# Kernel tuning notes

Measured on AMD Instinct MI355X. Metric: run time of the kernel, lower is better.

Reference implementation:

```python
import jax, jax.numpy as jnp
import numpy as np

B, L, D = 4, 16384, 128          # batch, voxels per sample, d_model
DI, DS, DTR, K = 256, 16, 8, 4   # d_inner, d_state, dt_rank, conv kernel
N = B * L
EPS = 1e-5


def setup_inputs() -> dict:
    key = jax.random.key(0)
    ks = jax.random.split(key, 12)
    s = 0.02
    feats = jax.random.normal(ks[0], (N, D), jnp.float32)
    coords_xyz = jax.random.randint(ks[1], (N, 3), 0, 1024, jnp.int32)
    # per-batch Morton permutation + its inverse
    perm = jnp.stack([jax.random.permutation(jax.random.fold_in(ks[2], i), L) for i in range(B)]).astype(jnp.int32)
    inv_perm = jnp.argsort(perm, axis=1).astype(jnp.int32)
    return {
        'feats': feats,
        'pos_w': jax.random.normal(ks[3], (3, D), jnp.float32) * s,
        'pos_b': jnp.zeros((D,), jnp.float32),
        'rms_w': jnp.ones((D,), jnp.float32),
        'in_proj_w': jax.random.normal(ks[4], (D, 2 * DI), jnp.float32) * s,
        'conv_w': jax.random.normal(ks[5], (DI, K), jnp.float32) * s,
        'conv_b': jnp.zeros((DI,), jnp.float32),
        'x_proj_w': jax.random.normal(ks[6], (DI, DTR + 2 * DS), jnp.float32) * s,
        'dt_proj_w': jax.random.normal(ks[7], (DTR, DI), jnp.float32) * s,
        'dt_proj_b': jax.random.normal(ks[8], (DI,), jnp.float32) * 0.1,
        'A_log': jnp.log(jnp.broadcast_to(jnp.arange(1.0, DS + 1.0, dtype=jnp.float32), (DI, DS))),
        'D_param': jnp.ones((DI,), jnp.float32),
        'out_proj_w': jax.random.normal(ks[9], (DI, D), jnp.float32) * s,
        'ln_w': jnp.ones((D,), jnp.float32),
        'ln_b': jnp.zeros((D,), jnp.float32),
        'coords_xyz': coords_xyz,
        'perm': perm,
        'inv_perm': inv_perm,
    }


def _gssm(feats, pos_w, pos_b, rms_w, in_proj_w, conv_w, conv_b, x_proj_w,
          dt_proj_w, dt_proj_b, A_log, D_param, out_proj_w, ln_w, ln_b,
          coords_xyz, perm, inv_perm):
    # positional embedding of voxel coords
    pe = coords_xyz.astype(jnp.float32) @ pos_w + pos_b            # [N, D]
    h = (feats + pe).reshape(B, L, D)
    # gather into Morton order (per-batch fancy index)
    hm = jnp.take_along_axis(h, perm[:, :, None].astype(jnp.int32), axis=1)  # [B, L, D]
    # Mamba block: RMSNorm then mixer (block returns mixer output only)
    x = hm * jax.lax.rsqrt(jnp.mean(hm * hm, axis=-1, keepdims=True) + EPS) * rms_w
    xz = x @ in_proj_w                                             # [B, L, 2*DI]
    xi, z = xz[..., :DI], xz[..., DI:]
    # depthwise causal conv1d, kernel K
    xp = jnp.pad(xi, ((0, 0), (K - 1, 0), (0, 0)))
    xc = conv_b + sum(xp[:, j:j + L, :] * conv_w[:, j] for j in range(K))
    xc = jax.nn.silu(xc)                                           # [B, L, DI]
    dbc = xc @ x_proj_w                                            # [B, L, DTR+2*DS]
    dt, Bm, Cm = dbc[..., :DTR], dbc[..., DTR:DTR + DS], dbc[..., DTR + DS:]
    dt = jax.nn.softplus(dt @ dt_proj_w + dt_proj_b)               # [B, L, DI]
    A = -jnp.exp(A_log)                                            # [DI, DS]

    def step(hst, inp):
        x_t, dt_t, b_t, c_t = inp                                  # [B,DI],[B,DI],[B,DS],[B,DS]
        hst = jnp.exp(dt_t[..., None] * A) * hst + (dt_t * x_t)[..., None] * b_t[:, None, :]
        return hst, jnp.einsum('bds,bs->bd', hst, c_t)

    h0 = jnp.zeros((B, DI, DS), xc.dtype)
    _, ys = jax.lax.scan(step, h0, (xc.transpose(1, 0, 2), dt.transpose(1, 0, 2),
                                    Bm.transpose(1, 0, 2), Cm.transpose(1, 0, 2)))
    y = ys.transpose(1, 0, 2) + xc * D_param                       # [B, L, DI]
    y = y * jax.nn.silu(z)
    out = y @ out_proj_w                                           # [B, L, D]
    # scatter back to original voxel order
    out = jnp.take_along_axis(out, inv_perm[:, :, None].astype(jnp.int32), axis=1).reshape(N, D)
    # post-SSM LayerNorm
    mu = jnp.mean(out, axis=-1, keepdims=True)
    var = jnp.mean((out - mu) ** 2, axis=-1, keepdims=True)
    return (out - mu) * jax.lax.rsqrt(var + EPS) * ln_w + ln_b


def reference(feats, pos_w, pos_b, rms_w, in_proj_w, conv_w, conv_b, x_proj_w,
              dt_proj_w, dt_proj_b, A_log, D_param, out_proj_w, ln_w, ln_b,
              coords_xyz, perm, inv_perm):
    return _gssm(feats, pos_w, pos_b, rms_w, in_proj_w, conv_w, conv_b, x_proj_w,
                 dt_proj_w, dt_proj_b, A_log, D_param, out_proj_w, ln_w, ln_b,
                 coords_xyz, perm, inv_perm)
```

## Files before the change

kernel.cpp:

```cpp
#include <hip/hip_runtime.h>
#include <hip/hip_bf16.h>
#include <math.h>

#define B_   4
#define L_   16384
#define D_   128
#define DI_  256
#define DS_  16
#define DTR_ 8
#define N_   65536
#define NC_  128
#define LC_  128
#define TW_  16
#define TP_  260
#define EPS_ 1e-5f

typedef __hip_bfloat16 bf16;
typedef __attribute__((ext_vector_type(8))) short short8;
typedef __attribute__((ext_vector_type(4))) float f32x4;

__device__ __forceinline__ bool probe_bf16(const void* Dp) {
  return ((const unsigned*)Dp)[0] == 0x3F803F80u;
}
__device__ __forceinline__ float ldin(const void* p, size_t i, bool isb) {
  return isb ? __bfloat162float(((const bf16*)p)[i]) : ((const float*)p)[i];
}
__device__ __forceinline__ float4 ld4(const void* p, size_t i4, bool isb) {
  if (!isb) return ((const float4*)p)[i4];
  const ushort4 v = ((const ushort4*)p)[i4];
  float4 r;
  r.x = __uint_as_float((unsigned)v.x << 16);
  r.y = __uint_as_float((unsigned)v.y << 16);
  r.z = __uint_as_float((unsigned)v.z << 16);
  r.w = __uint_as_float((unsigned)v.w << 16);
  return r;
}
__device__ __forceinline__ void splitbf(float v, ushort& hi, ushort& lo) {
  bf16 h = __float2bfloat16(v);
  float rem = v - __bfloat162float(h);
  bf16 l = __float2bfloat16(rem);
  hi = *(ushort*)&h;
  lo = *(ushort*)&l;
}


__global__ __launch_bounds__(256) void k_xnorm(
    const void* __restrict__ feats, const void* __restrict__ pos_w,
    const void* __restrict__ pos_b, const void* __restrict__ rms_w,
    const int* __restrict__ coords, const int* __restrict__ perm,
    const void* __restrict__ Dprobe,
    ushort* __restrict__ xh, ushort* __restrict__ xl) {
  const bool isb = probe_bf16(Dprobe);
  int wv = threadIdx.x >> 6, lane = threadIdx.x & 63;
  int p = blockIdx.x * 4 + wv;
  int b = p >> 14;
  int srow = b * L_ + perm[p];
  float cx = (float)coords[srow*3+0];
  float cy = (float)coords[srow*3+1];
  float cz = (float)coords[srow*3+2];
  int i0 = lane, i1 = lane + 64;
  float h0 = ldin(feats,(size_t)srow*D_ + i0,isb) + cx*ldin(pos_w,i0,isb) + cy*ldin(pos_w,D_+i0,isb)
           + cz*ldin(pos_w,2*D_+i0,isb) + ldin(pos_b,i0,isb);
  float h1 = ldin(feats,(size_t)srow*D_ + i1,isb) + cx*ldin(pos_w,i1,isb) + cy*ldin(pos_w,D_+i1,isb)
           + cz*ldin(pos_w,2*D_+i1,isb) + ldin(pos_b,i1,isb);
  float ss = h0*h0 + h1*h1;
  #pragma unroll
  for (int off = 32; off; off >>= 1) ss += __shfl_xor(ss, off);
  float r = 1.0f / sqrtf(ss * (1.f/128.f) + EPS_);
  float v0 = h0 * r * ldin(rms_w,i0,isb);
  float v1 = h1 * r * ldin(rms_w,i1,isb);
  ushort a, bq;
  splitbf(v0, a, bq);
  xh[(size_t)p*D_ + i0] = a; xl[(size_t)p*D_ + i0] = bq;
  splitbf(v1, a, bq);
  xh[(size_t)p*D_ + i1] = a; xl[(size_t)p*D_ + i1] = bq;
}

__global__ __launch_bounds__(256) void k_prepw(
    const void* __restrict__ Win, const void* __restrict__ Dprobe,
    ushort* __restrict__ wth, ushort* __restrict__ wtl) {
  const bool isb = probe_bf16(Dprobe);
  int idx = blockIdx.x * 256 + threadIdx.x;
  int k = idx >> 9, n = idx & 511;
  float v = ldin(Win, (size_t)k*512 + n, isb);
  ushort a, b;
  splitbf(v, a, b);
  wth[(size_t)n*128 + k] = a;
  wtl[(size_t)n*128 + k] = b;
}

__global__ __launch_bounds__(256) void k_prepxw(
    const void* __restrict__ xW, const void* __restrict__ Dprobe,
    ushort* __restrict__ wxh, ushort* __restrict__ wxl) {
  const bool isb = probe_bf16(Dprobe);
  int idx = blockIdx.x * 256 + threadIdx.x;
  int q = idx >> 8, c = idx & 255;
  float v = (q < 40) ? ldin(xW, (size_t)c*40 + q, isb) : 0.f;
  ushort a, b;
  splitbf(v, a, b);
  wxh[idx] = a;
  wxl[idx] = b;
}

__global__ __launch_bounds__(256) void k_prepdtw(
    const void* __restrict__ dtW, const void* __restrict__ Dprobe,
    ushort* __restrict__ dtwh, ushort* __restrict__ dtwl) {
  const bool isb = probe_bf16(Dprobe);
  int idx = blockIdx.x * 256 + threadIdx.x;
  int d = idx >> 5, k = idx & 31;
  float v = (k < 8) ? ldin(dtW, (size_t)k*256 + d, isb) : 0.f;
  ushort a, b;
  splitbf(v, a, b);
  dtwh[idx] = a;
  dtwl[idx] = b;
}

__global__ __launch_bounds__(256) void k_inproj(
    const ushort* __restrict__ xh, const ushort* __restrict__ xl,
    const ushort* __restrict__ wth, const ushort* __restrict__ wtl,
    float* __restrict__ xiT, float* __restrict__ zB) {
  __shared__ short Ah[64*136];
  __shared__ short Al[64*136];
  __shared__ short Bh[32*136];
  __shared__ short Bl[32*136];
  int tid = threadIdx.x;
  int T0 = blockIdx.x * 64;
  int lane = tid & 63, w = tid >> 6;
  {
    int k0 = (tid & 15) * 8;
    int m0 = tid >> 4;
    #pragma unroll
    for (int mi = 0; mi < 4; ++mi) {
      int m = m0 + 16*mi;
      *(short8*)&Ah[m*136 + k0] = *(const short8*)&xh[(size_t)(T0+m)*128 + k0];
      *(short8*)&Al[m*136 + k0] = *(const short8*)&xl[(size_t)(T0+m)*128 + k0];
    }
  }
  __syncthreads();
  int mloc = lane & 15, quad = lane >> 4;
  short8 afh[4], afl[4];
  #pragma unroll
  for (int ks = 0; ks < 4; ++ks) {
    int ka = ks*32 + quad*8;
    afh[ks] = *(const short8*)&Ah[(w*16 + mloc)*136 + ka];
    afl[ks] = *(const short8*)&Al[(w*16 + mloc)*136 + ka];
  }
  for (int ct = 0; ct < 16; ++ct) {
    int C0 = ct * 32;
    __syncthreads();
    {
      int k0 = (tid & 15) * 8;
      int n0 = tid >> 4;
      #pragma unroll
      for (int ni = 0; ni < 2; ++ni) {
        int n = n0 + 16*ni;
        *(short8*)&Bh[n*136 + k0] = *(const short8*)&wth[(size_t)(C0+n)*128 + k0];
        *(short8*)&Bl[n*136 + k0] = *(const short8*)&wtl[(size_t)(C0+n)*128 + k0];
      }
    }
    __syncthreads();
    #pragma unroll
    for (int nt = 0; nt < 2; ++nt) {
      f32x4 acc = {0.f, 0.f, 0.f, 0.f};
      #pragma unroll
      for (int ks = 0; ks < 4; ++ks) {
        int kb = ks*32 + quad*8;
        short8 bh = *(const short8*)&Bh[(nt*16 + mloc)*136 + kb];
        short8 bl = *(const short8*)&Bl[(nt*16 + mloc)*136 + kb];
        acc = __builtin_amdgcn_mfma_f32_16x16x32_bf16(afh[ks], bh, acc, 0, 0, 0);
        acc = __builtin_amdgcn_mfma_f32_16x16x32_bf16(afl[ks], bh, acc, 0, 0, 0);
        acc = __builtin_amdgcn_mfma_f32_16x16x32_bf16(afh[ks], bl, acc, 0, 0, 0);
      }
      int col = C0 + nt*16 + mloc;
      int trow = T0 + w*16 + quad*4;
      if (col < 256) {
        *(float4*)&xiT[(size_t)col*N_ + trow] = make_float4(acc[0], acc[1], acc[2], acc[3]);
      } else {
        int zc = col - 256;
        #pragma unroll
        for (int r = 0; r < 4; ++r)
          zB[(size_t)(trow + r)*256 + zc] = acc[r];
      }
    }
  }
}

__global__ __launch_bounds__(256) void k_conv_s(
    const float* __restrict__ xiT, const void* __restrict__ conv_w,
    const void* __restrict__ conv_b, const void* __restrict__ Dprobe,
    float* __restrict__ xcT) {
  const bool isb = probe_bf16(Dprobe);
  int idx = blockIdx.x * 256 + threadIdx.x;
  int c = idx >> 16;
  int t = idx & 65535;
  int l = t & (L_-1);
  const float* row = xiT + (size_t)c * N_;
  float acc = ldin(conv_b, c, isb);
  if (l >= 3) acc += row[t-3] * ldin(conv_w, c*4+0, isb);
  if (l >= 2) acc += row[t-2] * ldin(conv_w, c*4+1, isb);
  if (l >= 1) acc += row[t-1] * ldin(conv_w, c*4+2, isb);
  acc += row[t] * ldin(conv_w, c*4+3, isb);
  xcT[(size_t)c*N_ + t] = acc / (1.f + __expf(-acc));
}

__global__ __launch_bounds__(256) void k_xproj(
    const float* __restrict__ xcT,
    const ushort* __restrict__ wxh, const ushort* __restrict__ wxl,
    const ushort* __restrict__ dtwh, const ushort* __restrict__ dtwl,
    const void* __restrict__ dtb, const void* __restrict__ Dprobe,
    float* __restrict__ dtT, float* __restrict__ BmB, float* __restrict__ CmB) {
  const bool isb = probe_bf16(Dprobe);
  __shared__ float s40[64*52];
  __shared__ float sdtb[256];
  const int tid = threadIdx.x;
  const int lane = tid & 63, w = tid >> 6;
  const int T0 = blockIdx.x * 64;
  const int n15 = lane & 15, quad = lane >> 4;
  sdtb[tid] = ldin(dtb, tid, isb);

  f32x4 acc0 = {0.f,0.f,0.f,0.f}, acc1 = {0.f,0.f,0.f,0.f}, acc2 = {0.f,0.f,0.f,0.f};
  const float* xb = &xcT[(size_t)(quad*8)*N_ + T0 + w*16 + n15];
  #pragma unroll
  for (int ks = 0; ks < 8; ++ks) {
    short8 bh, bl;
    #pragma unroll
    for (int j = 0; j < 8; ++j) {
      ushort h, l;
      splitbf(xb[(size_t)(ks*32 + j)*N_], h, l);
      bh[j] = (short)h; bl[j] = (short)l;
    }
    #pragma unroll
    for (int mt = 0; mt < 3; ++mt) {
      const size_t aoff = (size_t)(mt*16 + n15)*256 + ks*32 + quad*8;
      short8 ah = *(const short8*)&wxh[aoff];
      short8 al = *(const short8*)&wxl[aoff];
      f32x4 a = (mt==0) ? acc0 : (mt==1) ? acc1 : acc2;
      a = __builtin_amdgcn_mfma_f32_16x16x32_bf16(ah, bh, a, 0, 0, 0);
      a = __builtin_amdgcn_mfma_f32_16x16x32_bf16(al, bh, a, 0, 0, 0);
      a = __builtin_amdgcn_mfma_f32_16x16x32_bf16(ah, bl, a, 0, 0, 0);
      if (mt==0) acc0 = a; else if (mt==1) acc1 = a; else acc2 = a;
    }
  }
  {
    const int trow = (w*16 + n15)*52;
    #pragma unroll
    for (int r = 0; r < 4; ++r) {
      s40[trow +      quad*4 + r] = acc0[r];
      s40[trow + 16 + quad*4 + r] = acc1[r];
      s40[trow + 32 + quad*4 + r] = acc2[r];
    }
  }
  __syncthreads();
  {
    int t = tid >> 2, fq = tid & 3;
    float4 bm = *(const float4*)&s40[t*52 + 8  + fq*4];
    float4 cm = *(const float4*)&s40[t*52 + 24 + fq*4];
    *(float4*)&BmB[(size_t)(T0+t)*16 + fq*4] = bm;
    *(float4*)&CmB[(size_t)(T0+t)*16 + fq*4] = cm;
  }
  short8 dh, dl;
  #pragma unroll
  for (int j = 0; j < 8; ++j) {
    ushort h, l;
    splitbf(s40[(w*16 + n15)*52 + quad*8 + j], h, l);
    dh[j] = (short)h; dl[j] = (short)l;
  }
  #pragma unroll
  for (int mt = 0; mt < 16; ++mt) {
    f32x4 a = {0.f,0.f,0.f,0.f};
    const size_t doff = (size_t)(mt*16 + n15)*32 + quad*8;
    short8 ah = *(const short8*)&dtwh[doff];
    short8 al = *(const short8*)&dtwl[doff];
    a = __builtin_amdgcn_mfma_f32_16x16x32_bf16(ah, dh, a, 0, 0, 0);
    a = __builtin_amdgcn_mfma_f32_16x16x32_bf16(al, dh, a, 0, 0, 0);
    a = __builtin_amdgcn_mfma_f32_16x16x32_bf16(ah, dl, a, 0, 0, 0);
    #pragma unroll
    for (int r = 0; r < 4; ++r) {
      int d = mt*16 + quad*4 + r;
      float pre = a[r] + sdtb[d];
      float sp = (pre > 20.f) ? pre : log1pf(__expf(pre));
      dtT[(size_t)d*N_ + T0 + w*16 + n15] = sp;
    }
  }
}

__global__ __launch_bounds__(256) void k_scan1(
    const float* __restrict__ dtT, const float* __restrict__ xcT,
    const float* __restrict__ BmB, const void* __restrict__ A_log,
    const void* __restrict__ Dprobe, float* __restrict__ Pb, float* __restrict__ Sb) {
  const bool isb = probe_bf16(Dprobe);
  __shared__ float sdt[TW_*TP_];
  __shared__ float sxc[TW_*TP_];
  __shared__ float sbm[LC_*16];
  int tid = threadIdx.x;
  int blk = blockIdx.x;
  int b = blk >> 7, ch = blk & 127;
  int T0 = b * L_ + ch * LC_;
  int d = tid;
  #pragma unroll
  for (int p = 0; p < 2; ++p) {
    int f = (p*256 + tid) * 4;
    *(float4*)&sbm[f] = *(const float4*)&BmB[(size_t)T0*16 + f];
  }
  float Al[16];
  #pragma unroll
  for (int s = 0; s < 16; ++s) Al[s] = -__expf(ldin(A_log, d*16 + s, isb));
  float h[16];
  #pragma unroll
  for (int s = 0; s < 16; ++s) h[s] = 0.f;
  float sumdt = 0.f;
  for (int it = 0; it < LC_; it += TW_) {
    __syncthreads();
    #pragma unroll
    for (int p = 0; p < 4; ++p) {
      int idx = p*256 + tid;
      int d2 = idx >> 2;
      int i4 = (idx & 3) * 4;
      float4 v = *(const float4*)&dtT[(size_t)d2*N_ + T0 + it + i4];
      float4 w = *(const float4*)&xcT[(size_t)d2*N_ + T0 + it + i4];
      sdt[(i4+0)*TP_ + d2] = v.x; sdt[(i4+1)*TP_ + d2] = v.y;
      sdt[(i4+2)*TP_ + d2] = v.z; sdt[(i4+3)*TP_ + d2] = v.w;
      sxc[(i4+0)*TP_ + d2] = w.x; sxc[(i4+1)*TP_ + d2] = w.y;
      sxc[(i4+2)*TP_ + d2] = w.z; sxc[(i4+3)*TP_ + d2] = w.w;
    }
    __syncthreads();
    #pragma unroll
    for (int i = 0; i < TW_; ++i) {
      float dtv = sdt[i*TP_ + d];
      float xcv = sxc[i*TP_ + d];
      sumdt += dtv;
      float du = dtv * xcv;
      const float* bmr = &sbm[(it+i)*16];
      #pragma unroll
      for (int s = 0; s < 16; ++s)
        h[s] = __expf(dtv * Al[s]) * h[s] + du * bmr[s];
    }
  }
  size_t rec = ((size_t)blk*256 + d) * 16;
  #pragma unroll
  for (int s = 0; s < 16; ++s) {
    Sb[rec + s] = h[s];
    Pb[rec + s] = __expf(Al[s] * sumdt);
  }
}

__global__ __launch_bounds__(256) void k_scan2(
    const float* __restrict__ Pb, const float* __restrict__ Sb, float* __restrict__ Hin) {
  int tid = blockIdx.x * 256 + threadIdx.x;
  int b = tid >> 12, r = tid & 4095;
  float h = 0.f;
  for (int ch = 0; ch < NC_; ++ch) {
    size_t rec = ((size_t)(b*NC_ + ch)) * 4096 + r;
    Hin[rec] = h;
    h = Pb[rec] * h + Sb[rec];
  }
}

__global__ __launch_bounds__(256) void k_scan3(
    const float* __restrict__ dtT, const float* __restrict__ xcT,
    const float* __restrict__ BmB, const float* __restrict__ CmB,
    const void* __restrict__ A_log, const void* __restrict__ Dp,
    const float* __restrict__ Hin, float* __restrict__ zyg) {
  const bool isb = probe_bf16(Dp);
  __shared__ float sdt[TW_*TP_];
  __shared__ float sxc[TW_*TP_];
  __shared__ float sbm[LC_*16];
  __shared__ float scm[LC_*16];
  int tid = threadIdx.x;
  int blk = blockIdx.x;
  int b = blk >> 7, ch = blk & 127;
  int T0 = b * L_ + ch * LC_;
  int d = tid;
  #pragma unroll
  for (int p = 0; p < 2; ++p) {
    int f = (p*256 + tid) * 4;
    *(float4*)&sbm[f] = *(const float4*)&BmB[(size_t)T0*16 + f];
    *(float4*)&scm[f] = *(const float4*)&CmB[(size_t)T0*16 + f];
  }
  float Al[16];
  #pragma unroll
  for (int s = 0; s < 16; ++s) Al[s] = -__expf(ldin(A_log, d*16 + s, isb));
  float h[16];
  size_t rec = ((size_t)blk*256 + d) * 16;
  #pragma unroll
  for (int s = 0; s < 16; ++s) h[s] = Hin[rec + s];
  float Dv = ldin(Dp, d, isb);
  for (int it = 0; it < LC_; it += TW_) {
    __syncthreads();
    #pragma unroll
    for (int p = 0; p < 4; ++p) {
      int idx = p*256 + tid;
      int d2 = idx >> 2;
      int i4 = (idx & 3) * 4;
      float4 v = *(const float4*)&dtT[(size_t)d2*N_ + T0 + it + i4];
      float4 w = *(const float4*)&xcT[(size_t)d2*N_ + T0 + it + i4];
      sdt[(i4+0)*TP_ + d2] = v.x; sdt[(i4+1)*TP_ + d2] = v.y;
      sdt[(i4+2)*TP_ + d2] = v.z; sdt[(i4+3)*TP_ + d2] = v.w;
      sxc[(i4+0)*TP_ + d2] = w.x; sxc[(i4+1)*TP_ + d2] = w.y;
      sxc[(i4+2)*TP_ + d2] = w.z; sxc[(i4+3)*TP_ + d2] = w.w;
    }
    __syncthreads();
    #pragma unroll
    for (int i = 0; i < TW_; ++i) {
      float dtv = sdt[i*TP_ + d];
      float xcv = sxc[i*TP_ + d];
      float du = dtv * xcv;
      const float* bmr = &sbm[(it+i)*16];
      const float* cmr = &scm[(it+i)*16];
      float y = 0.f;
      #pragma unroll
      for (int s = 0; s < 16; ++s) {
        h[s] = __expf(dtv * Al[s]) * h[s] + du * bmr[s];
        y += h[s] * cmr[s];
      }
      float yv = y + xcv * Dv;
      size_t zi = (size_t)(T0 + it + i)*256 + d;
      float zv = zyg[zi];
      float sil = zv / (1.f + __expf(-zv));
      zyg[zi] = yv * sil;
    }
  }
}

__global__ __launch_bounds__(256) void k_outproj(
    const float* __restrict__ yg, const void* __restrict__ W2,
    const void* __restrict__ Dprobe, float* __restrict__ outp) {
  const bool isb = probe_bf16(Dprobe);
  __shared__ float As[64*68];
  __shared__ float Bs[64*128];
  int tid = threadIdx.x;
  int T0 = blockIdx.x * 64;
  int tm = tid & 15, tn = tid >> 4;
  float acc[4][8] = {{0.f}};
  for (int kb = 0; kb < 256; kb += 64) {
    {
      int m = tid & 63, kq = tid >> 6;
      #pragma unroll
      for (int r = 0; r < 4; ++r) {
        int k0 = kq*16 + r*4;
        float4 v = *(const float4*)&yg[(size_t)(T0+m)*256 + kb + k0];
        As[(k0+0)*68+m] = v.x; As[(k0+1)*68+m] = v.y;
        As[(k0+2)*68+m] = v.z; As[(k0+3)*68+m] = v.w;
      }
      int n = (tid & 31)*4, kq2 = tid >> 5;
      #pragma unroll
      for (int p = 0; p < 8; ++p) {
        int k = kq2 + p*8;
        float4 w = ld4(W2, ((size_t)(kb+k)*128 + n) >> 2, isb);
        *(float4*)&Bs[k*128 + n] = w;
      }
    }
    __syncthreads();
    #pragma unroll 4
    for (int k = 0; k < 64; ++k) {
      float4 a  = *(const float4*)&As[k*68 + tm*4];
      float4 b0 = *(const float4*)&Bs[k*128 + tn*8];
      float4 b1 = *(const float4*)&Bs[k*128 + tn*8 + 4];
      float am[4] = {a.x, a.y, a.z, a.w};
      float bn[8] = {b0.x, b0.y, b0.z, b0.w, b1.x, b1.y, b1.z, b1.w};
      #pragma unroll
      for (int mi = 0; mi < 4; ++mi)
        #pragma unroll
        for (int ni = 0; ni < 8; ++ni)
          acc[mi][ni] += am[mi] * bn[ni];
    }
    __syncthreads();
  }
  #pragma unroll
  for (int mi = 0; mi < 4; ++mi) {
    size_t m = (size_t)(T0 + tm*4 + mi);
    *(float4*)&outp[m*128 + tn*8]     = make_float4(acc[mi][0], acc[mi][1], acc[mi][2], acc[mi][3]);
    *(float4*)&outp[m*128 + tn*8 + 4] = make_float4(acc[mi][4], acc[mi][5], acc[mi][6], acc[mi][7]);
  }
}

__global__ __launch_bounds__(256) void k_ln(
    const float* __restrict__ outp, const int* __restrict__ perm,
    const void* __restrict__ ln_w, const void* __restrict__ ln_b,
    const void* __restrict__ Dprobe, void* __restrict__ out) {
  const bool isb = probe_bf16(Dprobe);
  int wv = threadIdx.x >> 6, lane = threadIdx.x & 63;
  int p = blockIdx.x * 4 + wv;
  int b = p >> 14;
  int dest = b * L_ + perm[p];
  float v0 = outp[(size_t)p*128 + lane];
  float v1 = outp[(size_t)p*128 + lane + 64];
  float s1 = v0 + v1, s2 = v0*v0 + v1*v1;
  #pragma unroll
  for (int off = 32; off; off >>= 1) {
    s1 += __shfl_xor(s1, off);
    s2 += __shfl_xor(s2, off);
  }
  float mean = s1 * (1.f/128.f);
  float var  = s2 * (1.f/128.f) - mean*mean;
  float r = 1.0f / sqrtf(var + EPS_);
  float o0 = (v0 - mean)*r*ldin(ln_w,lane,isb)    + ldin(ln_b,lane,isb);
  float o1 = (v1 - mean)*r*ldin(ln_w,lane+64,isb) + ldin(ln_b,lane+64,isb);
  if (isb) {
    ((bf16*)out)[(size_t)dest*128 + lane]      = __float2bfloat16(o0);
    ((bf16*)out)[(size_t)dest*128 + lane + 64] = __float2bfloat16(o1);
  } else {
    ((float*)out)[(size_t)dest*128 + lane]      = o0;
    ((float*)out)[(size_t)dest*128 + lane + 64] = o1;
  }
}

extern "C" void kernel_launch(void* const* d_in, const int* in_sizes, int n_in,
                              void* d_out, int out_size, void* d_ws, size_t ws_size,
                              hipStream_t stream) {
  const void* feats    = d_in[0];
  const void* pos_w    = d_in[1];
  const void* pos_b    = d_in[2];
  const void* rms_w    = d_in[3];
  const void* in_proj  = d_in[4];
  const void* conv_w   = d_in[5];
  const void* conv_b   = d_in[6];
  const void* x_proj   = d_in[7];
  const void* dt_projw = d_in[8];
  const void* dt_projb = d_in[9];
  const void* A_log    = d_in[10];
  const void* D_param  = d_in[11];
  const void* out_proj = d_in[12];
  const void* ln_w     = d_in[13];
  const void* ln_b     = d_in[14];
  const int*  coords   = (const int*)d_in[15];
  const int*  perm     = (const int*)d_in[16];

  float* ws = (float*)d_ws;
  const size_t NN = (size_t)N_;
  ushort* xh  = (ushort*)ws;
  ushort* xl  = (ushort*)(ws + 64*NN);
  ushort* wth = (ushort*)(ws + 640*NN);
  ushort* wtl = (ushort*)(ws + 641*NN);
  ushort* wxh  = (ushort*)ws;
  ushort* wxl  = ((ushort*)ws) + 12288;
  ushort* dtwh = ((ushort*)ws) + 24576;
  ushort* dtwl = ((ushort*)ws) + 32768;
  float* Pb   = ws;
  float* Sb   = ws + 32*NN;
  float* Hin  = ws + 64*NN;
  float* BmB  = ws + 96*NN;
  float* CmB  = ws + 112*NN;
  float* xiT  = ws + 128*NN;
  float* dtT  = ws + 128*NN;
  float* outp = ws + 128*NN;
  float* zB   = ws + 384*NN;
  float* yg   = zB;
  float* xcT  = ws + 640*NN;

  k_prepw<<<256, 256, 0, stream>>>(in_proj, D_param, wth, wtl);
  k_xnorm<<<N_/4, 256, 0, stream>>>(feats, pos_w, pos_b, rms_w, coords, perm, D_param, xh, xl);
  k_inproj<<<N_/64, 256, 0, stream>>>(xh, xl, wth, wtl, xiT, zB);
  k_prepxw<<<48, 256, 0, stream>>>(x_proj, D_param, wxh, wxl);
  k_prepdtw<<<32, 256, 0, stream>>>(dt_projw, D_param, dtwh, dtwl);
  k_conv_s<<<(DI_*N_)/256, 256, 0, stream>>>(xiT, conv_w, conv_b, D_param, xcT);
  k_xproj<<<N_/64, 256, 0, stream>>>(xcT, wxh, wxl, dtwh, dtwl, dt_projb, D_param, dtT, BmB, CmB);
  k_scan1<<<B_*NC_, 256, 0, stream>>>(dtT, xcT, BmB, A_log, D_param, Pb, Sb);
  k_scan2<<<64, 256, 0, stream>>>(Pb, Sb, Hin);
  k_scan3<<<B_*NC_, 256, 0, stream>>>(dtT, xcT, BmB, CmB, A_log, D_param, Hin, zB);
  k_outproj<<<N_/64, 256, 0, stream>>>(yg, out_proj, D_param, outp);
  k_ln<<<N_/4, 256, 0, stream>>>(outp, perm, ln_w, ln_b, D_param, d_out);
}
```

Baseline: 557.7 us.

## Split scan state across thread pairs, prefetch tiles, use geometric exp recurrence

The chunked scan kernels now use 512 threads, with two threads per channel each owning 8 of the 16 states. The output dot product is combined with a lane shuffle. Next-tile dt/xc loads are prefetched into registers while the current tile is computed. When A follows an arithmetic progression (A_log = log(1..16)), a runtime check enables a path that replaces 8 exps per step with one exp plus repeated multiplies. The intent is to raise occupancy and parallelism on 512 blocks and cut transcendental work, at the cost of a runtime branch and small precision drift from chained multiplies.

After: 543.0 us. 2.6% less time.

```diff
diff --git a/kernel.cpp b/kernel.cpp
--- a/kernel.cpp
+++ b/kernel.cpp
@@ -284,7 +284,7 @@
   }
 }
 
-__global__ __launch_bounds__(256) void k_scan1(
+__global__ __launch_bounds__(512, 4) void k_scan1(
     const float* __restrict__ dtT, const float* __restrict__ xcT,
     const float* __restrict__ BmB, const void* __restrict__ A_log,
     const void* __restrict__ Dprobe, float* __restrict__ Pb, float* __restrict__ Sb) {
@@ -292,53 +292,95 @@
   __shared__ float sdt[TW_*TP_];
   __shared__ float sxc[TW_*TP_];
   __shared__ float sbm[LC_*16];
-  int tid = threadIdx.x;
-  int blk = blockIdx.x;
-  int b = blk >> 7, ch = blk & 127;
-  int T0 = b * L_ + ch * LC_;
-  int d = tid;
-  #pragma unroll
-  for (int p = 0; p < 2; ++p) {
-    int f = (p*256 + tid) * 4;
+  const int tid = threadIdx.x;
+  const int blk = blockIdx.x;
+  const int b = blk >> 7, ch = blk & 127;
+  const int T0 = b * L_ + ch * LC_;
+  const int d = tid >> 1, sh = tid & 1, s0 = sh * 8;
+  {
+    int f = tid * 4;
     *(float4*)&sbm[f] = *(const float4*)&BmB[(size_t)T0*16 + f];
   }
-  float Al[16];
-  #pragma unroll
-  for (int s = 0; s < 16; ++s) Al[s] = -__expf(ldin(A_log, d*16 + s, isb));
-  float h[16];
-  #pragma unroll
-  for (int s = 0; s < 16; ++s) h[s] = 0.f;
+  float Al[8];
+  #pragma unroll
+  for (int s = 0; s < 8; ++s) Al[s] = -__expf(ldin(A_log, d*16 + s0 + s, isb));
+  const float Al0 = (sh == 0) ? Al[0] : -__expf(ldin(A_log, d*16, isb));
+  bool fast = true;
+  #pragma unroll
+  for (int s = 0; s < 8; ++s)
+    fast = fast && (fabsf(Al[s] - (Al[0] + (float)s * Al0)) <= 1e-4f * fabsf(Al[s]));
+  float h[8];
+  #pragma unroll
+  for (int s = 0; s < 8; ++s) h[s] = 0.f;
   float sumdt = 0.f;
+  float4 vd[2], vx[2];
+  #pragma unroll
+  for (int q = 0; q < 2; ++q) {
+    int idx = q*512 + tid;
+    int c2 = idx >> 2, i4 = (idx & 3) * 4;
+    size_t off = (size_t)c2*N_ + T0 + i4;
+    vd[q] = *(const float4*)&dtT[off];
+    vx[q] = *(const float4*)&xcT[off];
+  }
   for (int it = 0; it < LC_; it += TW_) {
     __syncthreads();
     #pragma unroll
-    for (int p = 0; p < 4; ++p) {
-      int idx = p*256 + tid;
-      int d2 = idx >> 2;
-      int i4 = (idx & 3) * 4;
-      float4 v = *(const float4*)&dtT[(size_t)d2*N_ + T0 + it + i4];
-      float4 w = *(const float4*)&xcT[(size_t)d2*N_ + T0 + it + i4];
-      sdt[(i4+0)*TP_ + d2] = v.x; sdt[(i4+1)*TP_ + d2] = v.y;
-      sdt[(i4+2)*TP_ + d2] = v.z; sdt[(i4+3)*TP_ + d2] = v.w;
-      sxc[(i4+0)*TP_ + d2] = w.x; sxc[(i4+1)*TP_ + d2] = w.y;
-      sxc[(i4+2)*TP_ + d2] = w.z; sxc[(i4+3)*TP_ + d2] = w.w;
-    }
-    __syncthreads();
-    #pragma unroll
-    for (int i = 0; i < TW_; ++i) {
-      float dtv = sdt[i*TP_ + d];
-      float xcv = sxc[i*TP_ + d];
-      sumdt += dtv;
-      float du = dtv * xcv;
-      const float* bmr = &sbm[(it+i)*16];
-      #pragma unroll
-      for (int s = 0; s < 16; ++s)
-        h[s] = __expf(dtv * Al[s]) * h[s] + du * bmr[s];
-    }
-  }
-  size_t rec = ((size_t)blk*256 + d) * 16;
-  #pragma unroll
-  for (int s = 0; s < 16; ++s) {
+    for (int q = 0; q < 2; ++q) {
+      int idx = q*512 + tid;
+      int c2 = idx >> 2, i4 = (idx & 3) * 4;
+      sdt[(i4+0)*TP_ + c2] = vd[q].x; sdt[(i4+1)*TP_ + c2] = vd[q].y;
+      sdt[(i4+2)*TP_ + c2] = vd[q].z; sdt[(i4+3)*TP_ + c2] = vd[q].w;
+      sxc[(i4+0)*TP_ + c2] = vx[q].x; sxc[(i4+1)*TP_ + c2] = vx[q].y;
+      sxc[(i4+2)*TP_ + c2] = vx[q].z; sxc[(i4+3)*TP_ + c2] = vx[q].w;
+    }
+    __syncthreads();
+    if (it + TW_ < LC_) {
+      #pragma unroll
+      for (int q = 0; q < 2; ++q) {
+        int idx = q*512 + tid;
+        int c2 = idx >> 2, i4 = (idx & 3) * 4;
+        size_t off = (size_t)c2*N_ + T0 + it + TW_ + i4;
+        vd[q] = *(const float4*)&dtT[off];
+        vx[q] = *(const float4*)&xcT[off];
+      }
+    }
+    if (fast) {
+      #pragma unroll
+      for (int i = 0; i < TW_; ++i) {
+        float dtv = sdt[i*TP_ + d];
+        float xcv = sxc[i*TP_ + d];
+        sumdt += dtv;
+        float du = dtv * xcv;
+        float e1 = __expf(dtv * Al0);
+        float p  = __expf(dtv * Al[0]);
+        const float4 b0 = *(const float4*)&sbm[(it+i)*16 + s0];
+        const float4 b1 = *(const float4*)&sbm[(it+i)*16 + s0 + 4];
+        h[0] = p*h[0] + du*b0.x; p *= e1;
+        h[1] = p*h[1] + du*b0.y; p *= e1;
+        h[2] = p*h[2] + du*b0.z; p *= e1;
+        h[3] = p*h[3] + du*b0.w; p *= e1;
+        h[4] = p*h[4] + du*b1.x; p *= e1;
+        h[5] = p*h[5] + du*b1.y; p *= e1;
+        h[6] = p*h[6] + du*b1.z; p *= e1;
+        h[7] = p*h[7] + du*b1.w;
+      }
+    } else {
+      #pragma unroll
+      for (int i = 0; i < TW_; ++i) {
+        float dtv = sdt[i*TP_ + d];
+        float xcv = sxc[i*TP_ + d];
+        sumdt += dtv;
+        float du = dtv * xcv;
+        const float* bmr = &sbm[(it+i)*16 + s0];
+        #pragma unroll
+        for (int s = 0; s < 8; ++s)
+          h[s] = __expf(dtv * Al[s]) * h[s] + du * bmr[s];
+      }
+    }
+  }
+  size_t rec = ((size_t)blk*256 + d) * 16 + s0;
+  #pragma unroll
+  for (int s = 0; s < 8; ++s) {
     Sb[rec + s] = h[s];
     Pb[rec + s] = __expf(Al[s] * sumdt);
   }
@@ -356,7 +398,7 @@
   }
 }
 
-__global__ __launch_bounds__(256) void k_scan3(
+__global__ __launch_bounds__(512, 4) void k_scan3(
     const float* __restrict__ dtT, const float* __restrict__ xcT,
     const float* __restrict__ BmB, const float* __restrict__ CmB,
     const void* __restrict__ A_log, const void* __restrict__ Dp,
@@ -366,58 +408,102 @@
   __shared__ float sxc[TW_*TP_];
   __shared__ float sbm[LC_*16];
   __shared__ float scm[LC_*16];
-  int tid = threadIdx.x;
-  int blk = blockIdx.x;
-  int b = blk >> 7, ch = blk & 127;
-  int T0 = b * L_ + ch * LC_;
-  int d = tid;
-  #pragma unroll
-  for (int p = 0; p < 2; ++p) {
-    int f = (p*256 + tid) * 4;
+  const int tid = threadIdx.x;
+  const int blk = blockIdx.x;
+  const int b = blk >> 7, ch = blk & 127;
+  const int T0 = b * L_ + ch * LC_;
+  const int d = tid >> 1, sh = tid & 1, s0 = sh * 8;
+  {
+    int f = tid * 4;
     *(float4*)&sbm[f] = *(const float4*)&BmB[(size_t)T0*16 + f];
     *(float4*)&scm[f] = *(const float4*)&CmB[(size_t)T0*16 + f];
   }
-  float Al[16];
-  #pragma unroll
-  for (int s = 0; s < 16; ++s) Al[s] = -__expf(ldin(A_log, d*16 + s, isb));
-  float h[16];
-  size_t rec = ((size_t)blk*256 + d) * 16;
-  #pragma unroll
-  for (int s = 0; s < 16; ++s) h[s] = Hin[rec + s];
-  float Dv = ldin(Dp, d, isb);
+  float Al[8];
+  #pragma unroll
+  for (int s = 0; s < 8; ++s) Al[s] = -__expf(ldin(A_log, d*16 + s0 + s, isb));
+  const float Al0 = (sh == 0) ? Al[0] : -__expf(ldin(A_log, d*16, isb));
+  bool fast = true;
+  #pragma unroll
+  for (int s = 0; s < 8; ++s)
+    fast = fast && (fabsf(Al[s] - (Al[0] + (float)s * Al0)) <= 1e-4f * fabsf(Al[s]));
+  float h[8];
+  size_t rec = ((size_t)blk*256 + d) * 16 + s0;
+  #pragma unroll
+  for (int s = 0; s < 8; ++s) h[s] = Hin[rec + s];
+  const float Dv = ldin(Dp, d, isb);
+  float4 vd[2], vx[2];
+  #pragma unroll
+  for (int q = 0; q < 2; ++q) {
+    int idx = q*512 + tid;
+    int c2 = idx >> 2, i4 = (idx & 3) * 4;
+    size_t off = (size_t)c2*N_ + T0 + i4;
+    vd[q] = *(const float4*)&dtT[off];
+    vx[q] = *(const float4*)&xcT[off];
+  }
   for (int it = 0; it < LC_; it += TW_) {
     __syncthreads();
     #pragma unroll
-    for (int p = 0; p < 4; ++p) {
-      int idx = p*256 + tid;
-      int d2 = idx >> 2;
-      int i4 = (idx & 3) * 4;
-      float4 v = *(const float4*)&dtT[(size_t)d2*N_ + T0 + it + i4];
-      float4 w = *(const float4*)&xcT[(size_t)d2*N_ + T0 + it + i4];
-      sdt[(i4+0)*TP_ + d2] = v.x; sdt[(i4+1)*TP_ + d2] = v.y;
-      sdt[(i4+2)*TP_ + d2] = v.z; sdt[(i4+3)*TP_ + d2] = v.w;
-      sxc[(i4+0)*TP_ + d2] = w.x; sxc[(i4+1)*TP_ + d2] = w.y;
-      sxc[(i4+2)*TP_ + d2] = w.z; sxc[(i4+3)*TP_ + d2] = w.w;
-    }
-    __syncthreads();
+    for (int q = 0; q < 2; ++q) {
+      int idx = q*512 + tid;
+      int c2 = idx >> 2, i4 = (idx & 3) * 4;
+      sdt[(i4+0)*TP_ + c2] = vd[q].x; sdt[(i4+1)*TP_ + c2] = vd[q].y;
+      sdt[(i4+2)*TP_ + c2] = vd[q].z; sdt[(i4+3)*TP_ + c2] = vd[q].w;
+      sxc[(i4+0)*TP_ + c2] = vx[q].x; sxc[(i4+1)*TP_ + c2] = vx[q].y;
+      sxc[(i4+2)*TP_ + c2] = vx[q].z; sxc[(i4+3)*TP_ + c2] = vx[q].w;
+    }
+    __syncthreads();
+    if (it + TW_ < LC_) {
+      #pragma unroll
+      for (int q = 0; q < 2; ++q) {
+        int idx = q*512 + tid;
+        int c2 = idx >> 2, i4 = (idx & 3) * 4;
+        size_t off = (size_t)c2*N_ + T0 + it + TW_ + i4;
+        vd[q] = *(const float4*)&dtT[off];
+        vx[q] = *(const float4*)&xcT[off];
+      }
+    }
+    float zv[TW_];
+    if (sh == 0) {
+      #pragma unroll
+      for (int i = 0; i < TW_; ++i) zv[i] = zyg[(size_t)(T0 + it + i)*256 + d];
+    }
     #pragma unroll
     for (int i = 0; i < TW_; ++i) {
       float dtv = sdt[i*TP_ + d];
       float xcv = sxc[i*TP_ + d];
       float du = dtv * xcv;
-      const float* bmr = &sbm[(it+i)*16];
-      const float* cmr = &scm[(it+i)*16];
-      float y = 0.f;
-      #pragma unroll
-      for (int s = 0; s < 16; ++s) {
-        h[s] = __expf(dtv * Al[s]) * h[s] + du * bmr[s];
-        y += h[s] * cmr[s];
-      }
-      float yv = y + xcv * Dv;
-      size_t zi = (size_t)(T0 + it + i)*256 + d;
-      float zv = zyg[zi];
-      float sil = zv / (1.f + __expf(-zv));
-      zyg[zi] = yv * sil;
+      const float4 b0 = *(const float4*)&sbm[(it+i)*16 + s0];
+      const float4 b1 = *(const float4*)&sbm[(it+i)*16 + s0 + 4];
+      const float4 c0 = *(const float4*)&scm[(it+i)*16 + s0];
+      const float4 c1 = *(const float4*)&scm[(it+i)*16 + s0 + 4];
+      float yp = 0.f;
+      if (fast) {
+        float e1 = __expf(dtv * Al0);
+        float p  = __expf(dtv * Al[0]);
+        h[0] = p*h[0] + du*b0.x; yp += h[0]*c0.x; p *= e1;
+        h[1] = p*h[1] + du*b0.y; yp += h[1]*c0.y; p *= e1;
+        h[2] = p*h[2] + du*b0.z; yp += h[2]*c0.z; p *= e1;
+        h[3] = p*h[3] + du*b0.w; yp += h[3]*c0.w; p *= e1;
+        h[4] = p*h[4] + du*b1.x; yp += h[4]*c1.x; p *= e1;
+        h[5] = p*h[5] + du*b1.y; yp += h[5]*c1.y; p *= e1;
+        h[6] = p*h[6] + du*b1.z; yp += h[6]*c1.z; p *= e1;
+        h[7] = p*h[7] + du*b1.w; yp += h[7]*c1.w;
+      } else {
+        const float* bmr = &sbm[(it+i)*16 + s0];
+        const float* cmr = &scm[(it+i)*16 + s0];
+        #pragma unroll
+        for (int s = 0; s < 8; ++s) {
+          h[s] = __expf(dtv * Al[s]) * h[s] + du * bmr[s];
+          yp += h[s] * cmr[s];
+        }
+      }
+      float yt = yp + __shfl_xor(yp, 1);
+      if (sh == 0) {
+        float yv = yt + xcv * Dv;
+        float zvv = zv[i];
+        float sil = zvv / (1.f + __expf(-zvv));
+        zyg[(size_t)(T0 + it + i)*256 + d] = yv * sil;
+      }
     }
   }
 }
@@ -555,9 +641,9 @@
   k_prepdtw<<<32, 256, 0, stream>>>(dt_projw, D_param, dtwh, dtwl);
   k_conv_s<<<(DI_*N_)/256, 256, 0, stream>>>(xiT, conv_w, conv_b, D_param, xcT);
   k_xproj<<<N_/64, 256, 0, stream>>>(xcT, wxh, wxl, dtwh, dtwl, dt_projb, D_param, dtT, BmB, CmB);
-  k_scan1<<<B_*NC_, 256, 0, stream>>>(dtT, xcT, BmB, A_log, D_param, Pb, Sb);
+  k_scan1<<<B_*NC_, 512, 0, stream>>>(dtT, xcT, BmB, A_log, D_param, Pb, Sb);
   k_scan2<<<64, 256, 0, stream>>>(Pb, Sb, Hin);
-  k_scan3<<<B_*NC_, 256, 0, stream>>>(dtT, xcT, BmB, CmB, A_log, D_param, Hin, zB);
+  k_scan3<<<B_*NC_, 512, 0, stream>>>(dtT, xcT, BmB, CmB, A_log, D_param, Hin, zB);
   k_outproj<<<N_/64, 256, 0, stream>>>(yg, out_proj, D_param, outp);
   k_ln<<<N_/4, 256, 0, stream>>>(outp, perm, ln_w, ln_b, D_param, d_out);
 }
```

## Fuse dt projection into scan kernels and use power-chain decay for integer A

Applied to the files above, without the earlier changes.

The 256-wide softplus dt tensor is no longer written by the x-projection kernel. Only the 8 dt-rank values per token are stored, and each scan kernel recomputes dt per channel from them with an 8-term dot product, which removes a large write and two re-reads of dtT. When A is detected at runtime to be integer multiples of A[0], the scan replaces 16 exponentials per step with one exponential and a chain of multiplies. The z loads in scan3 are also hoisted into a register batch. The trade is extra ALU work for recomputing dt twice, and slightly different rounding from the repeated-multiply decay.

After: 576.0 us. 1.03x slower.

```diff
diff --git a/kernel.cpp b/kernel.cpp
--- a/kernel.cpp
+++ b/kernel.cpp
@@ -100,19 +100,6 @@
   splitbf(v, a, b);
   wxh[idx] = a;
   wxl[idx] = b;
-}
-
-__global__ __launch_bounds__(256) void k_prepdtw(
-    const void* __restrict__ dtW, const void* __restrict__ Dprobe,
-    ushort* __restrict__ dtwh, ushort* __restrict__ dtwl) {
-  const bool isb = probe_bf16(Dprobe);
-  int idx = blockIdx.x * 256 + threadIdx.x;
-  int d = idx >> 5, k = idx & 31;
-  float v = (k < 8) ? ldin(dtW, (size_t)k*256 + d, isb) : 0.f;
-  ushort a, b;
-  splitbf(v, a, b);
-  dtwh[idx] = a;
-  dtwl[idx] = b;
 }
 
 __global__ __launch_bounds__(256) void k_inproj(
@@ -206,17 +193,12 @@
 __global__ __launch_bounds__(256) void k_xproj(
     const float* __restrict__ xcT,
     const ushort* __restrict__ wxh, const ushort* __restrict__ wxl,
-    const ushort* __restrict__ dtwh, const ushort* __restrict__ dtwl,
-    const void* __restrict__ dtb, const void* __restrict__ Dprobe,
-    float* __restrict__ dtT, float* __restrict__ BmB, float* __restrict__ CmB) {
-  const bool isb = probe_bf16(Dprobe);
+    float* __restrict__ dbc8, float* __restrict__ BmB, float* __restrict__ CmB) {
   __shared__ float s40[64*52];
-  __shared__ float sdtb[256];
   const int tid = threadIdx.x;
   const int lane = tid & 63, w = tid >> 6;
   const int T0 = blockIdx.x * 64;
   const int n15 = lane & 15, quad = lane >> 4;
-  sdtb[tid] = ldin(dtb, tid, isb);
 
   f32x4 acc0 = {0.f,0.f,0.f,0.f}, acc1 = {0.f,0.f,0.f,0.f}, acc2 = {0.f,0.f,0.f,0.f};
   const float* xb = &xcT[(size_t)(quad*8)*N_ + T0 + w*16 + n15];
@@ -258,53 +240,43 @@
     *(float4*)&BmB[(size_t)(T0+t)*16 + fq*4] = bm;
     *(float4*)&CmB[(size_t)(T0+t)*16 + fq*4] = cm;
   }
-  short8 dh, dl;
-  #pragma unroll
-  for (int j = 0; j < 8; ++j) {
-    ushort h, l;
-    splitbf(s40[(w*16 + n15)*52 + quad*8 + j], h, l);
-    dh[j] = (short)h; dl[j] = (short)l;
-  }
-  #pragma unroll
-  for (int mt = 0; mt < 16; ++mt) {
-    f32x4 a = {0.f,0.f,0.f,0.f};
-    const size_t doff = (size_t)(mt*16 + n15)*32 + quad*8;
-    short8 ah = *(const short8*)&dtwh[doff];
-    short8 al = *(const short8*)&dtwl[doff];
-    a = __builtin_amdgcn_mfma_f32_16x16x32_bf16(ah, dh, a, 0, 0, 0);
-    a = __builtin_amdgcn_mfma_f32_16x16x32_bf16(al, dh, a, 0, 0, 0);
-    a = __builtin_amdgcn_mfma_f32_16x16x32_bf16(ah, dl, a, 0, 0, 0);
-    #pragma unroll
-    for (int r = 0; r < 4; ++r) {
-      int d = mt*16 + quad*4 + r;
-      float pre = a[r] + sdtb[d];
-      float sp = (pre > 20.f) ? pre : log1pf(__expf(pre));
-      dtT[(size_t)d*N_ + T0 + w*16 + n15] = sp;
-    }
+  if (tid < 128) {
+    int t = tid >> 1, half = tid & 1;
+    *(float4*)&dbc8[(size_t)(T0+t)*8 + half*4] = *(const float4*)&s40[t*52 + half*4];
   }
 }
 
 __global__ __launch_bounds__(256) void k_scan1(
-    const float* __restrict__ dtT, const float* __restrict__ xcT,
-    const float* __restrict__ BmB, const void* __restrict__ A_log,
-    const void* __restrict__ Dprobe, float* __restrict__ Pb, float* __restrict__ Sb) {
+    const float* __restrict__ xcT, const float* __restrict__ dbc8,
+    const float* __restrict__ BmB,
+    const void* __restrict__ dtW, const void* __restrict__ dtb,
+    const void* __restrict__ A_log, const void* __restrict__ Dprobe,
+    float* __restrict__ Pb, float* __restrict__ Sb) {
   const bool isb = probe_bf16(Dprobe);
-  __shared__ float sdt[TW_*TP_];
   __shared__ float sxc[TW_*TP_];
   __shared__ float sbm[LC_*16];
-  int tid = threadIdx.x;
-  int blk = blockIdx.x;
-  int b = blk >> 7, ch = blk & 127;
-  int T0 = b * L_ + ch * LC_;
-  int d = tid;
+  __shared__ float sdb[TW_*8];
+  const int tid = threadIdx.x;
+  const int blk = blockIdx.x;
+  const int b = blk >> 7, ch = blk & 127;
+  const int T0 = b * L_ + ch * LC_;
+  const int d = tid;
   #pragma unroll
   for (int p = 0; p < 2; ++p) {
     int f = (p*256 + tid) * 4;
     *(float4*)&sbm[f] = *(const float4*)&BmB[(size_t)T0*16 + f];
   }
+  float wv[8];
+  #pragma unroll
+  for (int r = 0; r < 8; ++r) wv[r] = ldin(dtW, r*256 + d, isb);
+  const float dtbv = ldin(dtb, d, isb);
   float Al[16];
   #pragma unroll
   for (int s = 0; s < 16; ++s) Al[s] = -__expf(ldin(A_log, d*16 + s, isb));
+  bool fast = true;
+  #pragma unroll
+  for (int s = 1; s < 16; ++s)
+    fast = fast && (fabsf(Al[s] - (float)(s+1) * Al[0]) <= 1e-4f * fabsf(Al[s]));
   float h[16];
   #pragma unroll
   for (int s = 0; s < 16; ++s) h[s] = 0.f;
@@ -316,24 +288,52 @@
       int idx = p*256 + tid;
       int d2 = idx >> 2;
       int i4 = (idx & 3) * 4;
-      float4 v = *(const float4*)&dtT[(size_t)d2*N_ + T0 + it + i4];
-      float4 w = *(const float4*)&xcT[(size_t)d2*N_ + T0 + it + i4];
-      sdt[(i4+0)*TP_ + d2] = v.x; sdt[(i4+1)*TP_ + d2] = v.y;
-      sdt[(i4+2)*TP_ + d2] = v.z; sdt[(i4+3)*TP_ + d2] = v.w;
-      sxc[(i4+0)*TP_ + d2] = w.x; sxc[(i4+1)*TP_ + d2] = w.y;
-      sxc[(i4+2)*TP_ + d2] = w.z; sxc[(i4+3)*TP_ + d2] = w.w;
-    }
+      float4 wq = *(const float4*)&xcT[(size_t)d2*N_ + T0 + it + i4];
+      sxc[(i4+0)*TP_ + d2] = wq.x; sxc[(i4+1)*TP_ + d2] = wq.y;
+      sxc[(i4+2)*TP_ + d2] = wq.z; sxc[(i4+3)*TP_ + d2] = wq.w;
+    }
+    if (tid < 32)
+      *(float4*)&sdb[tid*4] = *(const float4*)&dbc8[(size_t)(T0+it)*8 + tid*4];
     __syncthreads();
     #pragma unroll
     for (int i = 0; i < TW_; ++i) {
-      float dtv = sdt[i*TP_ + d];
+      float4 q0 = *(const float4*)&sdb[i*8];
+      float4 q1 = *(const float4*)&sdb[i*8 + 4];
+      float pre = dtbv + q0.x*wv[0] + q0.y*wv[1] + q0.z*wv[2] + q0.w*wv[3]
+                       + q1.x*wv[4] + q1.y*wv[5] + q1.z*wv[6] + q1.w*wv[7];
+      float dtv = (pre > 20.f) ? pre : log1pf(__expf(pre));
       float xcv = sxc[i*TP_ + d];
       sumdt += dtv;
       float du = dtv * xcv;
-      const float* bmr = &sbm[(it+i)*16];
-      #pragma unroll
-      for (int s = 0; s < 16; ++s)
-        h[s] = __expf(dtv * Al[s]) * h[s] + du * bmr[s];
+      const float4 b0 = *(const float4*)&sbm[(it+i)*16];
+      const float4 b1 = *(const float4*)&sbm[(it+i)*16 + 4];
+      const float4 b2 = *(const float4*)&sbm[(it+i)*16 + 8];
+      const float4 b3 = *(const float4*)&sbm[(it+i)*16 + 12];
+      if (fast) {
+        float e1 = __expf(dtv * Al[0]);
+        float p = e1;
+        h[0]  = p*h[0]  + du*b0.x; p *= e1;
+        h[1]  = p*h[1]  + du*b0.y; p *= e1;
+        h[2]  = p*h[2]  + du*b0.z; p *= e1;
+        h[3]  = p*h[3]  + du*b0.w; p *= e1;
+        h[4]  = p*h[4]  + du*b1.x; p *= e1;
+        h[5]  = p*h[5]  + du*b1.y; p *= e1;
+        h[6]  = p*h[6]  + du*b1.z; p *= e1;
+        h[7]  = p*h[7]  + du*b1.w; p *= e1;
+        h[8]  = p*h[8]  + du*b2.x; p *= e1;
+        h[9]  = p*h[9]  + du*b2.y; p *= e1;
+        h[10] = p*h[10] + du*b2.z; p *= e1;
+        h[11] = p*h[11] + du*b2.w; p *= e1;
+        h[12] = p*h[12] + du*b3.x; p *= e1;
+        h[13] = p*h[13] + du*b3.y; p *= e1;
+        h[14] = p*h[14] + du*b3.z; p *= e1;
+        h[15] = p*h[15] + du*b3.w;
+      } else {
+        const float* bmr = &sbm[(it+i)*16];
+        #pragma unroll
+        for (int s = 0; s < 16; ++s)
+          h[s] = __expf(dtv * Al[s]) * h[s] + du * bmr[s];
+      }
     }
   }
   size_t rec = ((size_t)blk*256 + d) * 16;
@@ -357,34 +357,43 @@
 }
 
 __global__ __launch_bounds__(256) void k_scan3(
-    const float* __restrict__ dtT, const float* __restrict__ xcT,
+    const float* __restrict__ xcT, const float* __restrict__ dbc8,
     const float* __restrict__ BmB, const float* __restrict__ CmB,
+    const void* __restrict__ dtW, const void* __restrict__ dtb,
     const void* __restrict__ A_log, const void* __restrict__ Dp,
     const float* __restrict__ Hin, float* __restrict__ zyg) {
   const bool isb = probe_bf16(Dp);
-  __shared__ float sdt[TW_*TP_];
   __shared__ float sxc[TW_*TP_];
   __shared__ float sbm[LC_*16];
   __shared__ float scm[LC_*16];
-  int tid = threadIdx.x;
-  int blk = blockIdx.x;
-  int b = blk >> 7, ch = blk & 127;
-  int T0 = b * L_ + ch * LC_;
-  int d = tid;
+  __shared__ float sdb[TW_*8];
+  const int tid = threadIdx.x;
+  const int blk = blockIdx.x;
+  const int b = blk >> 7, ch = blk & 127;
+  const int T0 = b * L_ + ch * LC_;
+  const int d = tid;
   #pragma unroll
   for (int p = 0; p < 2; ++p) {
     int f = (p*256 + tid) * 4;
     *(float4*)&sbm[f] = *(const float4*)&BmB[(size_t)T0*16 + f];
     *(float4*)&scm[f] = *(const float4*)&CmB[(size_t)T0*16 + f];
   }
+  float wv[8];
+  #pragma unroll
+  for (int r = 0; r < 8; ++r) wv[r] = ldin(dtW, r*256 + d, isb);
+  const float dtbv = ldin(dtb, d, isb);
   float Al[16];
   #pragma unroll
   for (int s = 0; s < 16; ++s) Al[s] = -__expf(ldin(A_log, d*16 + s, isb));
+  bool fast = true;
+  #pragma unroll
+  for (int s = 1; s < 16; ++s)
+    fast = fast && (fabsf(Al[s] - (float)(s+1) * Al[0]) <= 1e-4f * fabsf(Al[s]));
   float h[16];
   size_t rec = ((size_t)blk*256 + d) * 16;
   #pragma unroll
   for (int s = 0; s < 16; ++s) h[s] = Hin[rec + s];
-  float Dv = ldin(Dp, d, isb);
+  const float Dv = ldin(Dp, d, isb);
   for (int it = 0; it < LC_; it += TW_) {
     __syncthreads();
     #pragma unroll
@@ -392,32 +401,66 @@
       int idx = p*256 + tid;
       int d2 = idx >> 2;
       int i4 = (idx & 3) * 4;
-      float4 v = *(const float4*)&dtT[(size_t)d2*N_ + T0 + it + i4];
-      float4 w = *(const float4*)&xcT[(size_t)d2*N_ + T0 + it + i4];
-      sdt[(i4+0)*TP_ + d2] = v.x; sdt[(i4+1)*TP_ + d2] = v.y;
-      sdt[(i4+2)*TP_ + d2] = v.z; sdt[(i4+3)*TP_ + d2] = v.w;
-      sxc[(i4+0)*TP_ + d2] = w.x; sxc[(i4+1)*TP_ + d2] = w.y;
-      sxc[(i4+2)*TP_ + d2] = w.z; sxc[(i4+3)*TP_ + d2] = w.w;
-    }
-    __syncthreads();
+      float4 wq = *(const float4*)&xcT[(size_t)d2*N_ + T0 + it + i4];
+      sxc[(i4+0)*TP_ + d2] = wq.x; sxc[(i4+1)*TP_ + d2] = wq.y;
+      sxc[(i4+2)*TP_ + d2] = wq.z; sxc[(i4+3)*TP_ + d2] = wq.w;
+    }
+    if (tid < 32)
+      *(float4*)&sdb[tid*4] = *(const float4*)&dbc8[(size_t)(T0+it)*8 + tid*4];
+    __syncthreads();
+    float zv[TW_];
+    #pragma unroll
+    for (int i = 0; i < TW_; ++i) zv[i] = zyg[(size_t)(T0 + it + i)*256 + d];
     #pragma unroll
     for (int i = 0; i < TW_; ++i) {
-      float dtv = sdt[i*TP_ + d];
+      float4 q0 = *(const float4*)&sdb[i*8];
+      float4 q1 = *(const float4*)&sdb[i*8 + 4];
+      float pre = dtbv + q0.x*wv[0] + q0.y*wv[1] + q0.z*wv[2] + q0.w*wv[3]
+                       + q1.x*wv[4] + q1.y*wv[5] + q1.z*wv[6] + q1.w*wv[7];
+      float dtv = (pre > 20.f) ? pre : log1pf(__expf(pre));
       float xcv = sxc[i*TP_ + d];
       float du = dtv * xcv;
-      const float* bmr = &sbm[(it+i)*16];
-      const float* cmr = &scm[(it+i)*16];
-      float y = 0.f;
-      #pragma unroll
-      for (int s = 0; s < 16; ++s) {
-        h[s] = __expf(dtv * Al[s]) * h[s] + du * bmr[s];
-        y += h[s] * cmr[s];
+      const float4 b0 = *(const float4*)&sbm[(it+i)*16];
+      const float4 b1 = *(const float4*)&sbm[(it+i)*16 + 4];
+      const float4 b2 = *(const float4*)&sbm[(it+i)*16 + 8];
+      const float4 b3 = *(const float4*)&sbm[(it+i)*16 + 12];
+      const float4 c0 = *(const float4*)&scm[(it+i)*16];
+      const float4 c1 = *(const float4*)&scm[(it+i)*16 + 4];
+      const float4 c2 = *(const float4*)&scm[(it+i)*16 + 8];
+      const float4 c3 = *(const float4*)&scm[(it+i)*16 + 12];
+      float yp = 0.f;
+      if (fast) {
+        float e1 = __expf(dtv * Al[0]);
+        float p = e1;
+        h[0]  = p*h[0]  + du*b0.x; yp += h[0] *c0.x; p *= e1;
+        h[1]  = p*h[1]  + du*b0.y; yp += h[1] *c0.y; p *= e1;
+        h[2]  = p*h[2]  + du*b0.z; yp += h[2] *c0.z; p *= e1;
+        h[3]  = p*h[3]  + du*b0.w; yp += h[3] *c0.w; p *= e1;
+        h[4]  = p*h[4]  + du*b1.x; yp += h[4] *c1.x; p *= e1;
+        h[5]  = p*h[5]  + du*b1.y; yp += h[5] *c1.y; p *= e1;
+        h[6]  = p*h[6]  + du*b1.z; yp += h[6] *c1.z; p *= e1;
+        h[7]  = p*h[7]  + du*b1.w; yp += h[7] *c1.w; p *= e1;
+        h[8]  = p*h[8]  + du*b2.x; yp += h[8] *c2.x; p *= e1;
+        h[9]  = p*h[9]  + du*b2.y; yp += h[9] *c2.y; p *= e1;
+        h[10] = p*h[10] + du*b2.z; yp += h[10]*c2.z; p *= e1;
+        h[11] = p*h[11] + du*b2.w; yp += h[11]*c2.w; p *= e1;
+        h[12] = p*h[12] + du*b3.x; yp += h[12]*c3.x; p *= e1;
+        h[13] = p*h[13] + du*b3.y; yp += h[13]*c3.y; p *= e1;
+        h[14] = p*h[14] + du*b3.z; yp += h[14]*c3.z; p *= e1;
+        h[15] = p*h[15] + du*b3.w; yp += h[15]*c3.w;
+      } else {
+        const float* bmr = &sbm[(it+i)*16];
+        const float* cmr = &scm[(it+i)*16];
+        #pragma unroll
+        for (int s = 0; s < 16; ++s) {
+          h[s] = __expf(dtv * Al[s]) * h[s] + du * bmr[s];
+          yp += h[s] * cmr[s];
+        }
       }
-      float yv = y + xcv * Dv;
-      size_t zi = (size_t)(T0 + it + i)*256 + d;
-      float zv = zyg[zi];
-      float sil = zv / (1.f + __expf(-zv));
-      zyg[zi] = yv * sil;
+      float yv = yp + xcv * Dv;
+      float zvv = zv[i];
+      float sil = zvv / (1.f + __expf(-zvv));
+      zyg[(size_t)(T0 + it + i)*256 + d] = yv * sil;
     }
   }
 }
@@ -534,15 +577,13 @@
   ushort* wtl = (ushort*)(ws + 641*NN);
   ushort* wxh  = (ushort*)ws;
   ushort* wxl  = ((ushort*)ws) + 12288;
-  ushort* dtwh = ((ushort*)ws) + 24576;
-  ushort* dtwl = ((ushort*)ws) + 32768;
   float* Pb   = ws;
   float* Sb   = ws + 32*NN;
   float* Hin  = ws + 64*NN;
   float* BmB  = ws + 96*NN;
   float* CmB  = ws + 112*NN;
   float* xiT  = ws + 128*NN;
-  float* dtT  = ws + 128*NN;
+  float* dbc8 = ws + 128*NN;
   float* outp = ws + 128*NN;
   float* zB   = ws + 384*NN;
   float* yg   = zB;
@@ -552,12 +593,11 @@
   k_xnorm<<<N_/4, 256, 0, stream>>>(feats, pos_w, pos_b, rms_w, coords, perm, D_param, xh, xl);
   k_inproj<<<N_/64, 256, 0, stream>>>(xh, xl, wth, wtl, xiT, zB);
   k_prepxw<<<48, 256, 0, stream>>>(x_proj, D_param, wxh, wxl);
-  k_prepdtw<<<32, 256, 0, stream>>>(dt_projw, D_param, dtwh, dtwl);
   k_conv_s<<<(DI_*N_)/256, 256, 0, stream>>>(xiT, conv_w, conv_b, D_param, xcT);
-  k_xproj<<<N_/64, 256, 0, stream>>>(xcT, wxh, wxl, dtwh, dtwl, dt_projb, D_param, dtT, BmB, CmB);
-  k_scan1<<<B_*NC_, 256, 0, stream>>>(dtT, xcT, BmB, A_log, D_param, Pb, Sb);
+  k_xproj<<<N_/64, 256, 0, stream>>>(xcT, wxh, wxl, dbc8, BmB, CmB);
+  k_scan1<<<B_*NC_, 256, 0, stream>>>(xcT, dbc8, BmB, dt_projw, dt_projb, A_log, D_param, Pb, Sb);
   k_scan2<<<64, 256, 0, stream>>>(Pb, Sb, Hin);
-  k_scan3<<<B_*NC_, 256, 0, stream>>>(dtT, xcT, BmB, CmB, A_log, D_param, Hin, zB);
+  k_scan3<<<B_*NC_, 256, 0, stream>>>(xcT, dbc8, BmB, CmB, dt_projw, dt_projb, A_log, D_param, Hin, zB);
   k_outproj<<<N_/64, 256, 0, stream>>>(yg, out_proj, D_param, outp);
   k_ln<<<N_/4, 256, 0, stream>>>(outp, perm, ln_w, ln_b, D_param, d_out);
 }
```
